# Kernel tuning notes

Measured on AMD Instinct MI355X. Metric: run time of the kernel, lower is better.

## Reference

```python
import jax, jax.numpy as jnp
import numpy as np

B, IN, OUT = 4096, 128, 128
C = 1.0                    # curvature of the Poincare ball
SQRT_C = 1.0
MIN_ENORM = 1e-15          # manifold.min_enorm
BALL_EPS = 1e-5            # projection margin for backproject
EPS32 = float(np.finfo(np.float32).eps)
CLAMP = 1.0 * float(np.log(2.0 / EPS32))   # clamping_factor * log(2/eps)
SMOOTH = 50.0              # smoothing_factor


def _project(y, axis):
    # project back onto the open ball of radius (1 - eps)/sqrt(c)
    norm = jnp.clip(jnp.linalg.norm(y, axis=axis, keepdims=True), MIN_ENORM)
    maxnorm = (1.0 - BALL_EPS) / SQRT_C
    return jnp.where(norm > maxnorm, y * (maxnorm / norm), y)


def _lambda(y, axis):
    # conformal factor lambda(y) = 2 / (1 - c ||y||^2)
    sq = jnp.sum(y * y, axis=axis, keepdims=True)
    return 2.0 / jnp.clip(1.0 - C * sq, EPS32)


def _mobius_add(u, v, axis):
    uv = jnp.sum(u * v, axis=axis, keepdims=True)
    uu = jnp.sum(u * u, axis=axis, keepdims=True)
    vv = jnp.sum(v * v, axis=axis, keepdims=True)
    num = (1.0 + 2.0 * C * uv + C * vv) * u + (1.0 - C * uu) * v
    den = 1.0 + 2.0 * C * uv + (C * C) * uu * vv
    return num / jnp.clip(den, EPS32)


def _smooth_clamp(x, lo, hi, beta):
    # smooth version of clamp; -> hard clamp as beta -> inf
    return lo + (jax.nn.softplus(beta * (x - lo)) - jax.nn.softplus(beta * (x - hi))) / beta


def setup_inputs() -> dict:
    key = jax.random.key(0)
    k1, k2, k3 = jax.random.split(key, 3)
    v = jax.random.normal(k1, (B, IN), dtype=jnp.float32)
    x = 0.7 * v / (1.0 + jnp.linalg.norm(v, axis=-1, keepdims=True))  # strictly inside ball
    weight = jax.random.normal(k2, (OUT, IN), dtype=jnp.float32) * 0.05
    b = jax.random.normal(k3, (OUT, IN), dtype=jnp.float32)
    bias = 0.1 * b / (1.0 + jnp.linalg.norm(b, axis=-1, keepdims=True))  # in-ball translations
    return {"x": x, "weight": weight, "bias": bias}


def reference(x, weight, bias):
    # ptransp_0(weight, bias) = (lambda_0 / lambda_bias) * weight = (1 - c||bias||^2) * weight
    lam_b = _lambda(bias, -1)                       # (out, 1)
    a = (2.0 / lam_b) * weight                      # (out, in) tangent normals at bias
    p = bias                                        # (out, in)

    u = -p.T[None, :, :]                            # (1, in, out)
    v = x[:, :, None]                               # (B, in, 1)
    sub = _mobius_add(u, v, axis=1)                 # (B, in, out) = (-p) (+) x
    sub = _project(sub, axis=1)                     # backproject

    suba = jnp.sum(sub * a.T[None, :, :], axis=1, keepdims=True)         # (B, 1, out)
    a_norm = jnp.clip(jnp.linalg.norm(a, axis=-1, keepdims=True), MIN_ENORM).T  # (1, out)

    asinh_arg = SQRT_C * _lambda(sub, 1) * suba / a_norm[None, :, :]     # (B, 1, out)
    asinh_arg = _smooth_clamp(asinh_arg, -CLAMP, CLAMP, SMOOTH)
    signed_dist = jnp.arcsinh(asinh_arg) / SQRT_C                        # (B, 1, out)

    res = _lambda(p, -1).T * a_norm * signed_dist[:, 0, :]               # (B, out)
    return res
```

## Files before the change

kernel.cpp:

```cpp
#include <hip/hip_runtime.h>
#include <math.h>

#define BB 16
#define NOUT 128
#define NIN 128
#define NTHREADS 256

__global__ __launch_bounds__(NTHREADS) void hyper_kernel(
    const float* __restrict__ x,
    const float* __restrict__ weight,
    const float* __restrict__ bias,
    float* __restrict__ out)
{
    __shared__ __align__(16) float sx[BB][NIN];
    __shared__ float svv[BB];

    const int tid = threadIdx.x;
    const int b0 = blockIdx.x * BB;

    {
        const float4* xg = (const float4*)(x + (size_t)b0 * NIN);
        float4* xs = (float4*)(&sx[0][0]);
        xs[tid] = xg[tid];
        xs[tid + NTHREADS] = xg[tid + NTHREADS];
    }
    __syncthreads();

    if (tid < 128) {
        const int r = tid >> 3, seg = tid & 7;
        float s = 0.f;
        const float4* xr = (const float4*)(&sx[r][seg * 16]);
        #pragma unroll
        for (int j = 0; j < 4; ++j) {
            float4 v = xr[j];
            s = fmaf(v.x, v.x, fmaf(v.y, v.y, fmaf(v.z, v.z, fmaf(v.w, v.w, s))));
        }
        s += __shfl_xor(s, 1);
        s += __shfl_xor(s, 2);
        s += __shfl_xor(s, 4);
        if (seg == 0) svv[r] = s;
    }

    const int o = tid & 127;
    const int rbase = (tid >> 7) * (BB / 2);

    const float4* w4 = (const float4*)(weight + (size_t)o * NIN);
    const float4* b4 = (const float4*)(bias + (size_t)o * NIN);

    float accb[BB / 2], accw[BB / 2];
    #pragma unroll
    for (int r = 0; r < BB / 2; ++r) { accb[r] = 0.f; accw[r] = 0.f; }
    float uu = 0.f, bw = 0.f, ww = 0.f;

    #pragma unroll 4
    for (int kc = 0; kc < NIN / 4; ++kc) {
        const float4 wv = w4[kc];
        const float4 bv = b4[kc];
        uu = fmaf(bv.x, bv.x, uu); uu = fmaf(bv.y, bv.y, uu);
        uu = fmaf(bv.z, bv.z, uu); uu = fmaf(bv.w, bv.w, uu);
        bw = fmaf(bv.x, wv.x, bw); bw = fmaf(bv.y, wv.y, bw);
        bw = fmaf(bv.z, wv.z, bw); bw = fmaf(bv.w, wv.w, bw);
        ww = fmaf(wv.x, wv.x, ww); ww = fmaf(wv.y, wv.y, ww);
        ww = fmaf(wv.z, wv.z, ww); ww = fmaf(wv.w, wv.w, ww);
        #pragma unroll
        for (int r = 0; r < BB / 2; ++r) {
            const float4 xv = *(const float4*)(&sx[rbase + r][kc * 4]);
            accb[r] = fmaf(xv.x, bv.x, accb[r]); accb[r] = fmaf(xv.y, bv.y, accb[r]);
            accb[r] = fmaf(xv.z, bv.z, accb[r]); accb[r] = fmaf(xv.w, bv.w, accb[r]);
            accw[r] = fmaf(xv.x, wv.x, accw[r]); accw[r] = fmaf(xv.y, wv.y, accw[r]);
            accw[r] = fmaf(xv.z, wv.z, accw[r]); accw[r] = fmaf(xv.w, wv.w, accw[r]);
        }
    }
    __syncthreads();

    const float EPS = 1.1920928955078125e-7f;
    const float CLAMPV = 16.635532333438687f;
    const float INV_SMOOTH = 1.f / 50.f;
    const float SMOOTHF = 50.f;
    const float MAXNORM = 1.f - 1e-5f;

    const float beta = 1.f - uu;
    const float beta_c = fmaxf(beta, EPS);
    const float a_norm = fmaxf(beta_c * sqrtf(ww), 1e-15f);
    const float ba = beta_c * bw;
    const float outcoef = (2.f / beta_c) * a_norm;
    const float inv_anorm = 1.f / a_norm;

    #pragma unroll
    for (int r = 0; r < BB / 2; ++r) {
        const float vv = svv[rbase + r];
        const float uv = -accb[r];
        const float dax = beta_c * accw[r];
        const float alpha = 1.f + 2.f * uv + vv;
        const float den = fmaxf(1.f + 2.f * uv + uu * vv, EPS);
        const float inv_den = 1.f / den;
        float suba = (beta * dax - alpha * ba) * inv_den;
        float ss = (alpha * alpha * uu + 2.f * alpha * beta * uv + beta * beta * vv)
                   * (inv_den * inv_den);
        const float nrm = fmaxf(sqrtf(fmaxf(ss, 0.f)), 1e-15f);
        if (nrm > MAXNORM) {
            const float sc = MAXNORM / nrm;
            suba *= sc;
            ss *= sc * sc;
        }
        const float lam_sub = 2.f / fmaxf(1.f - ss, EPS);
        const float arg = lam_sub * suba * inv_anorm;
        const float t1 = SMOOTHF * (arg + CLAMPV);
        const float t2 = SMOOTHF * (arg - CLAMPV);
        const float sp1 = fmaxf(t1, 0.f) + log1pf(expf(-fabsf(t1)));
        const float sp2 = fmaxf(t2, 0.f) + log1pf(expf(-fabsf(t2)));
        const float scl = -CLAMPV + (sp1 - sp2) * INV_SMOOTH;
        const float sd = asinhf(scl);
        out[(size_t)(b0 + rbase + r) * NOUT + o] = outcoef * sd;
    }
}

extern "C" void kernel_launch(void* const* d_in, const int* in_sizes, int n_in,
                              void* d_out, int out_size, void* d_ws, size_t ws_size,
                              hipStream_t stream) {
    const float* x = (const float*)d_in[0];
    const float* w = (const float*)d_in[1];
    const float* b = (const float*)d_in[2];
    float* out = (float*)d_out;
    const int B = in_sizes[0] / NIN;
    dim3 grid(B / BB), block(NTHREADS);
    hipLaunchKernelGGL(hyper_kernel, grid, block, 0, stream, x, w, b, out);
}
```

Baseline: 79.00 us.

## Shrink rows per block, read x via scalar loads, split weight stats across halves

Cuts rows per block from 16 to 4, so the grid grows from 256 to 1024 blocks and fills more compute units. The shared-memory staging of x is dropped: each half-block reads its two x rows straight from global memory through a wave-uniform pointer (readfirstlane), which enables scalar loads. The per-output bias/weight norms are now computed only by the first half and passed through shared memory. The trade-off is that weight and bias are re-read by four times as many blocks, raising L2 traffic in exchange for parallelism and fewer redundant FMAs.

```diff
diff --git a/kernel.cpp b/kernel.cpp
--- a/kernel.cpp
+++ b/kernel.cpp
@@ -1,77 +1,92 @@
 #include <hip/hip_runtime.h>
 #include <math.h>
 
-#define BB 16
+#define NIN 128
 #define NOUT 128
-#define NIN 128
-#define NTHREADS 256
+#define BB 4
+#define NTH 256
 
-__global__ __launch_bounds__(NTHREADS) void hyper_kernel(
+template <bool STATS>
+__device__ __forceinline__ void dot_loop(
+    const float4* __restrict__ w4, const float4* __restrict__ b4,
+    const float* __restrict__ xr0, const float* __restrict__ xr1,
+    float& acb0, float& acw0, float& acb1, float& acw1,
+    float& uu, float& bw, float& ww)
+{
+    #pragma unroll
+    for (int kc = 0; kc < NIN / 4; ++kc) {
+        const float4 wv = w4[kc];
+        const float4 bv = b4[kc];
+        if (STATS) {
+            uu = fmaf(bv.x, bv.x, uu); uu = fmaf(bv.y, bv.y, uu);
+            uu = fmaf(bv.z, bv.z, uu); uu = fmaf(bv.w, bv.w, uu);
+            bw = fmaf(bv.x, wv.x, bw); bw = fmaf(bv.y, wv.y, bw);
+            bw = fmaf(bv.z, wv.z, bw); bw = fmaf(bv.w, wv.w, bw);
+            ww = fmaf(wv.x, wv.x, ww); ww = fmaf(wv.y, wv.y, ww);
+            ww = fmaf(wv.z, wv.z, ww); ww = fmaf(wv.w, wv.w, ww);
+        }
+        const float x00 = xr0[kc * 4 + 0], x01 = xr0[kc * 4 + 1];
+        const float x02 = xr0[kc * 4 + 2], x03 = xr0[kc * 4 + 3];
+        const float x10 = xr1[kc * 4 + 0], x11 = xr1[kc * 4 + 1];
+        const float x12 = xr1[kc * 4 + 2], x13 = xr1[kc * 4 + 3];
+        acb0 = fmaf(x00, bv.x, acb0); acb0 = fmaf(x01, bv.y, acb0);
+        acb0 = fmaf(x02, bv.z, acb0); acb0 = fmaf(x03, bv.w, acb0);
+        acw0 = fmaf(x00, wv.x, acw0); acw0 = fmaf(x01, wv.y, acw0);
+        acw0 = fmaf(x02, wv.z, acw0); acw0 = fmaf(x03, wv.w, acw0);
+        acb1 = fmaf(x10, bv.x, acb1); acb1 = fmaf(x11, bv.y, acb1);
+        acb1 = fmaf(x12, bv.z, acb1); acb1 = fmaf(x13, bv.w, acb1);
+        acw1 = fmaf(x10, wv.x, acw1); acw1 = fmaf(x11, wv.y, acw1);
+        acw1 = fmaf(x12, wv.z, acw1); acw1 = fmaf(x13, wv.w, acw1);
+    }
+}
+
+__global__ __launch_bounds__(NTH) void hyper_kernel(
     const float* __restrict__ x,
     const float* __restrict__ weight,
     const float* __restrict__ bias,
     float* __restrict__ out)
 {
-    __shared__ __align__(16) float sx[BB][NIN];
     __shared__ float svv[BB];
+    __shared__ float s_uu[NOUT];
+    __shared__ float s_bw[NOUT];
+    __shared__ float s_ww[NOUT];
 
     const int tid = threadIdx.x;
     const int b0 = blockIdx.x * BB;
+    const int o = tid & (NOUT - 1);
+    const int rh = tid >> 7;
 
-    {
-        const float4* xg = (const float4*)(x + (size_t)b0 * NIN);
-        float4* xs = (float4*)(&sx[0][0]);
-        xs[tid] = xg[tid];
-        xs[tid + NTHREADS] = xg[tid + NTHREADS];
-    }
-    __syncthreads();
-
-    if (tid < 128) {
-        const int r = tid >> 3, seg = tid & 7;
-        float s = 0.f;
-        const float4* xr = (const float4*)(&sx[r][seg * 16]);
-        #pragma unroll
-        for (int j = 0; j < 4; ++j) {
-            float4 v = xr[j];
-            s = fmaf(v.x, v.x, fmaf(v.y, v.y, fmaf(v.z, v.z, fmaf(v.w, v.w, s))));
-        }
+    if (tid < 32 * BB) {
+        const int r = tid >> 5, seg = tid & 31;
+        const float4 v = *(const float4*)(x + (size_t)(b0 + r) * NIN + seg * 4);
+        float s = fmaf(v.x, v.x, fmaf(v.y, v.y, fmaf(v.z, v.z, v.w * v.w)));
         s += __shfl_xor(s, 1);
         s += __shfl_xor(s, 2);
         s += __shfl_xor(s, 4);
+        s += __shfl_xor(s, 8);
+        s += __shfl_xor(s, 16);
         if (seg == 0) svv[r] = s;
     }
 
-    const int o = tid & 127;
-    const int rbase = (tid >> 7) * (BB / 2);
-
+    const int row0 = b0 + rh * 2;
+    const float* xr0 = x + (size_t)((unsigned)__builtin_amdgcn_readfirstlane(row0)) * NIN;
+    const float* xr1 = xr0 + NIN;
     const float4* w4 = (const float4*)(weight + (size_t)o * NIN);
     const float4* b4 = (const float4*)(bias + (size_t)o * NIN);
 
-    float accb[BB / 2], accw[BB / 2];
-    #pragma unroll
-    for (int r = 0; r < BB / 2; ++r) { accb[r] = 0.f; accw[r] = 0.f; }
+    float acb0 = 0.f, acw0 = 0.f, acb1 = 0.f, acw1 = 0.f;
     float uu = 0.f, bw = 0.f, ww = 0.f;
 
-    #pragma unroll 4
-    for (int kc = 0; kc < NIN / 4; ++kc) {
-        const float4 wv = w4[kc];
-        const float4 bv = b4[kc];
-        uu = fmaf(bv.x, bv.x, uu); uu = fmaf(bv.y, bv.y, uu);
-        uu = fmaf(bv.z, bv.z, uu); uu = fmaf(bv.w, bv.w, uu);
-        bw = fmaf(bv.x, wv.x, bw); bw = fmaf(bv.y, wv.y, bw);
-        bw = fmaf(bv.z, wv.z, bw); bw = fmaf(bv.w, wv.w, bw);
-        ww = fmaf(wv.x, wv.x, ww); ww = fmaf(wv.y, wv.y, ww);
-        ww = fmaf(wv.z, wv.z, ww); ww = fmaf(wv.w, wv.w, ww);
-        #pragma unroll
-        for (int r = 0; r < BB / 2; ++r) {
-            const float4 xv = *(const float4*)(&sx[rbase + r][kc * 4]);
-            accb[r] = fmaf(xv.x, bv.x, accb[r]); accb[r] = fmaf(xv.y, bv.y, accb[r]);
-            accb[r] = fmaf(xv.z, bv.z, accb[r]); accb[r] = fmaf(xv.w, bv.w, accb[r]);
-            accw[r] = fmaf(xv.x, wv.x, accw[r]); accw[r] = fmaf(xv.y, wv.y, accw[r]);
-            accw[r] = fmaf(xv.z, wv.z, accw[r]); accw[r] = fmaf(xv.w, wv.w, accw[r]);
-        }
+    if (rh == 0) {
+        dot_loop<true>(w4, b4, xr0, xr1, acb0, acw0, acb1, acw1, uu, bw, ww);
+        s_uu[o] = uu; s_bw[o] = bw; s_ww[o] = ww;
+    } else {
+        dot_loop<false>(w4, b4, xr0, xr1, acb0, acw0, acb1, acw1, uu, bw, ww);
     }
     __syncthreads();
+    uu = s_uu[o]; bw = s_bw[o]; ww = s_ww[o];
+    const float vv0 = svv[rh * 2 + 0];
+    const float vv1 = svv[rh * 2 + 1];
 
     const float EPS = 1.1920928955078125e-7f;
     const float CLAMPV = 16.635532333438687f;
@@ -86,9 +101,13 @@
     const float outcoef = (2.f / beta_c) * a_norm;
     const float inv_anorm = 1.f / a_norm;
 
+    float accb[2] = {acb0, acb1};
+    float accw[2] = {acw0, acw1};
+    float vvs[2] = {vv0, vv1};
+
     #pragma unroll
-    for (int r = 0; r < BB / 2; ++r) {
-        const float vv = svv[rbase + r];
+    for (int r = 0; r < 2; ++r) {
+        const float vv = vvs[r];
         const float uv = -accb[r];
         const float dax = beta_c * accw[r];
         const float alpha = 1.f + 2.f * uv + vv;
@@ -111,7 +130,7 @@
         const float sp2 = fmaxf(t2, 0.f) + log1pf(expf(-fabsf(t2)));
         const float scl = -CLAMPV + (sp1 - sp2) * INV_SMOOTH;
         const float sd = asinhf(scl);
-        out[(size_t)(b0 + rbase + r) * NOUT + o] = outcoef * sd;
+        out[(size_t)(row0 + r) * NOUT + o] = outcoef * sd;
     }
 }
 
@@ -123,6 +142,6 @@
     const float* b = (const float*)d_in[2];
     float* out = (float*)d_out;
     const int B = in_sizes[0] / NIN;
-    dim3 grid(B / BB), block(NTHREADS);
+    dim3 grid(B / BB), block(NTH);
     hipLaunchKernelGGL(hyper_kernel, grid, block, 0, stream, x, w, b, out);
 }
```

After: 101.7 us. 1.29x slower.

## Split K across 16-lane groups with DPP reductions and spread epilogue across lanes

Applied to the files above, without the earlier changes.

Restructures the kernel so that each 16-lane group owns one output column. The 128-wide dot products are split across the 16 lanes, 8 elements each, and summed with DPP row-rotate reductions. The transcendental-heavy epilogue is then distributed so each lane handles a different row, instead of one thread doing every row serially. Shared memory staging is removed: x is read straight from global memory and hits L2 repeatedly across the 8 column blocks. The grid grows to 1024 blocks. The cost is much more redundant global/L2 traffic for x and the extra reduction instructions.

```diff
diff --git a/kernel.cpp b/kernel.cpp
--- a/kernel.cpp
+++ b/kernel.cpp
@@ -1,84 +1,98 @@
 #include <hip/hip_runtime.h>
 #include <math.h>
 
-#define BB 16
+#define NIN 128
 #define NOUT 128
-#define NIN 128
-#define NTHREADS 256
+#define ROWS_PER_BLOCK 32
+#define COLS_PER_BLOCK 16
+#define NTH 256
 
-__global__ __launch_bounds__(NTHREADS) void hyper_kernel(
-    const float* __restrict__ x,
-    const float* __restrict__ weight,
-    const float* __restrict__ bias,
-    float* __restrict__ out)
+template <int N>
+__device__ __forceinline__ float row_ror(float v) {
+    return __int_as_float(__builtin_amdgcn_update_dpp(
+        0, __float_as_int(v), 0x120 + N, 0xF, 0xF, true));
+}
+
+__device__ __forceinline__ float red16(float v) {
+    v += row_ror<1>(v);
+    v += row_ror<2>(v);
+    v += row_ror<4>(v);
+    v += row_ror<8>(v);
+    return v;
+}
+
+__device__ __forceinline__ float dot8(float4 a0, float4 a1, float4 b0, float4 b1) {
+    float s = a0.x * b0.x;
+    s = fmaf(a0.y, b0.y, s);
+    s = fmaf(a0.z, b0.z, s);
+    s = fmaf(a0.w, b0.w, s);
+    s = fmaf(a1.x, b1.x, s);
+    s = fmaf(a1.y, b1.y, s);
+    s = fmaf(a1.z, b1.z, s);
+    s = fmaf(a1.w, b1.w, s);
+    return s;
+}
+
+__device__ __forceinline__ float epilogue(
+    float uv, float xw, float vv,
+    float uu, float beta, float beta_c, float ba,
+    float inv_anorm, float outcoef)
 {
-    __shared__ __align__(16) float sx[BB][NIN];
-    __shared__ float svv[BB];
-
-    const int tid = threadIdx.x;
-    const int b0 = blockIdx.x * BB;
-
-    {
-        const float4* xg = (const float4*)(x + (size_t)b0 * NIN);
-        float4* xs = (float4*)(&sx[0][0]);
-        xs[tid] = xg[tid];
-        xs[tid + NTHREADS] = xg[tid + NTHREADS];
-    }
-    __syncthreads();
-
-    if (tid < 128) {
-        const int r = tid >> 3, seg = tid & 7;
-        float s = 0.f;
-        const float4* xr = (const float4*)(&sx[r][seg * 16]);
-        #pragma unroll
-        for (int j = 0; j < 4; ++j) {
-            float4 v = xr[j];
-            s = fmaf(v.x, v.x, fmaf(v.y, v.y, fmaf(v.z, v.z, fmaf(v.w, v.w, s))));
-        }
-        s += __shfl_xor(s, 1);
-        s += __shfl_xor(s, 2);
-        s += __shfl_xor(s, 4);
-        if (seg == 0) svv[r] = s;
-    }
-
-    const int o = tid & 127;
-    const int rbase = (tid >> 7) * (BB / 2);
-
-    const float4* w4 = (const float4*)(weight + (size_t)o * NIN);
-    const float4* b4 = (const float4*)(bias + (size_t)o * NIN);
-
-    float accb[BB / 2], accw[BB / 2];
-    #pragma unroll
-    for (int r = 0; r < BB / 2; ++r) { accb[r] = 0.f; accw[r] = 0.f; }
-    float uu = 0.f, bw = 0.f, ww = 0.f;
-
-    #pragma unroll 4
-    for (int kc = 0; kc < NIN / 4; ++kc) {
-        const float4 wv = w4[kc];
-        const float4 bv = b4[kc];
-        uu = fmaf(bv.x, bv.x, uu); uu = fmaf(bv.y, bv.y, uu);
-        uu = fmaf(bv.z, bv.z, uu); uu = fmaf(bv.w, bv.w, uu);
-        bw = fmaf(bv.x, wv.x, bw); bw = fmaf(bv.y, wv.y, bw);
-        bw = fmaf(bv.z, wv.z, bw); bw = fmaf(bv.w, wv.w, bw);
-        ww = fmaf(wv.x, wv.x, ww); ww = fmaf(wv.y, wv.y, ww);
-        ww = fmaf(wv.z, wv.z, ww); ww = fmaf(wv.w, wv.w, ww);
-        #pragma unroll
-        for (int r = 0; r < BB / 2; ++r) {
-            const float4 xv = *(const float4*)(&sx[rbase + r][kc * 4]);
-            accb[r] = fmaf(xv.x, bv.x, accb[r]); accb[r] = fmaf(xv.y, bv.y, accb[r]);
-            accb[r] = fmaf(xv.z, bv.z, accb[r]); accb[r] = fmaf(xv.w, bv.w, accb[r]);
-            accw[r] = fmaf(xv.x, wv.x, accw[r]); accw[r] = fmaf(xv.y, wv.y, accw[r]);
-            accw[r] = fmaf(xv.z, wv.z, accw[r]); accw[r] = fmaf(xv.w, wv.w, accw[r]);
-        }
-    }
-    __syncthreads();
-
     const float EPS = 1.1920928955078125e-7f;
     const float CLAMPV = 16.635532333438687f;
     const float INV_SMOOTH = 1.f / 50.f;
     const float SMOOTHF = 50.f;
     const float MAXNORM = 1.f - 1e-5f;
 
+    const float dax = beta_c * xw;
+    const float alpha = 1.f + 2.f * uv + vv;
+    const float den = fmaxf(1.f + 2.f * uv + uu * vv, EPS);
+    const float inv_den = 1.f / den;
+    float suba = (beta * dax - alpha * ba) * inv_den;
+    float ss = (alpha * alpha * uu + 2.f * alpha * beta * uv + beta * beta * vv)
+               * (inv_den * inv_den);
+    const float nrm = fmaxf(sqrtf(fmaxf(ss, 0.f)), 1e-15f);
+    if (nrm > MAXNORM) {
+        const float sc = MAXNORM / nrm;
+        suba *= sc;
+        ss *= sc * sc;
+    }
+    const float lam_sub = 2.f / fmaxf(1.f - ss, EPS);
+    const float arg = lam_sub * suba * inv_anorm;
+    const float t1 = SMOOTHF * (arg + CLAMPV);
+    const float t2 = SMOOTHF * (arg - CLAMPV);
+    const float sp1 = fmaxf(t1, 0.f) + log1pf(expf(-fabsf(t1)));
+    const float sp2 = fmaxf(t2, 0.f) + log1pf(expf(-fabsf(t2)));
+    const float scl = -CLAMPV + (sp1 - sp2) * INV_SMOOTH;
+    return outcoef * asinhf(scl);
+}
+
+__global__ __launch_bounds__(NTH) void hyper_kernel(
+    const float* __restrict__ x,
+    const float* __restrict__ weight,
+    const float* __restrict__ bias,
+    float* __restrict__ out)
+{
+    const int tid = threadIdx.x;
+    const int wave = tid >> 6;
+    const int lane = tid & 63;
+    const int g = lane >> 4;
+    const int t = lane & 15;
+    const int blk_col = blockIdx.x & 7;
+    const int blk_row = blockIdx.x >> 3;
+    const int o = blk_col * COLS_PER_BLOCK + wave * 4 + g;
+    const int rb = blk_row * ROWS_PER_BLOCK;
+
+    const float4* wp = (const float4*)(weight + (size_t)o * NIN + t * 8);
+    const float4* bp = (const float4*)(bias + (size_t)o * NIN + t * 8);
+    const float4 wr0 = wp[0], wr1 = wp[1];
+    const float4 br0 = bp[0], br1 = bp[1];
+
+    const float uu = red16(dot8(br0, br1, br0, br1));
+    const float bw = red16(dot8(br0, br1, wr0, wr1));
+    const float ww = red16(dot8(wr0, wr1, wr0, wr1));
+
+    const float EPS = 1.1920928955078125e-7f;
     const float beta = 1.f - uu;
     const float beta_c = fmaxf(beta, EPS);
     const float a_norm = fmaxf(beta_c * sqrtf(ww), 1e-15f);
@@ -86,32 +100,27 @@
     const float outcoef = (2.f / beta_c) * a_norm;
     const float inv_anorm = 1.f / a_norm;
 
+    const float* xbase = x + (size_t)rb * NIN + t * 8;
+
     #pragma unroll
-    for (int r = 0; r < BB / 2; ++r) {
-        const float vv = svv[rbase + r];
-        const float uv = -accb[r];
-        const float dax = beta_c * accw[r];
-        const float alpha = 1.f + 2.f * uv + vv;
-        const float den = fmaxf(1.f + 2.f * uv + uu * vv, EPS);
-        const float inv_den = 1.f / den;
-        float suba = (beta * dax - alpha * ba) * inv_den;
-        float ss = (alpha * alpha * uu + 2.f * alpha * beta * uv + beta * beta * vv)
-                   * (inv_den * inv_den);
-        const float nrm = fmaxf(sqrtf(fmaxf(ss, 0.f)), 1e-15f);
-        if (nrm > MAXNORM) {
-            const float sc = MAXNORM / nrm;
-            suba *= sc;
-            ss *= sc * sc;
+    for (int c = 0; c < ROWS_PER_BLOCK / 16; ++c) {
+        float uvK = 0.f, xwK = 0.f, vvK = 0.f;
+        #pragma unroll 4
+        for (int r = 0; r < 16; ++r) {
+            const float4* xp = (const float4*)(xbase + (size_t)(c * 16 + r) * NIN);
+            const float4 xv0 = xp[0];
+            const float4 xv1 = xp[1];
+            float pb = dot8(xv0, xv1, br0, br1);
+            float pw = dot8(xv0, xv1, wr0, wr1);
+            float pv = dot8(xv0, xv1, xv0, xv1);
+            pb = red16(pb);
+            pw = red16(pw);
+            pv = red16(pv);
+            if (t == r) { uvK = -pb; xwK = pw; vvK = pv; }
         }
-        const float lam_sub = 2.f / fmaxf(1.f - ss, EPS);
-        const float arg = lam_sub * suba * inv_anorm;
-        const float t1 = SMOOTHF * (arg + CLAMPV);
-        const float t2 = SMOOTHF * (arg - CLAMPV);
-        const float sp1 = fmaxf(t1, 0.f) + log1pf(expf(-fabsf(t1)));
-        const float sp2 = fmaxf(t2, 0.f) + log1pf(expf(-fabsf(t2)));
-        const float scl = -CLAMPV + (sp1 - sp2) * INV_SMOOTH;
-        const float sd = asinhf(scl);
-        out[(size_t)(b0 + rbase + r) * NOUT + o] = outcoef * sd;
+        const float val = epilogue(uvK, xwK, vvK, uu, beta, beta_c, ba,
+                                   inv_anorm, outcoef);
+        out[(size_t)(rb + c * 16 + t) * NOUT + o] = val;
     }
 }
 
@@ -123,6 +132,6 @@
     const float* b = (const float*)d_in[2];
     float* out = (float*)d_out;
     const int B = in_sizes[0] / NIN;
-    dim3 grid(B / BB), block(NTHREADS);
+    dim3 grid((NOUT / COLS_PER_BLOCK) * (B / ROWS_PER_BLOCK)), block(NTH);
     hipLaunchKernelGGL(hyper_kernel, grid, block, 0, stream, x, w, b, out);
 }
```

Measured after the change: 77.98 us. No clear change (-1.3%).

## Use split-bf16 MFMA for x·W and x·b dot products with a prep kernel

Applied to the files above, without the earlier changes.

Adds a prep kernel that splits x, weight and bias into bf16 hi/lo pairs and precomputes the row norms of x and the per-output-column constants. The main kernel then computes x·W and x·b with 16x16x32 bf16 MFMA, using three products (hi·hi, hi·lo, lo·hi) to approximate fp32 accuracy, and runs the same elementwise hyperbolic epilogue as before. This replaces the scalar FMA inner loop and the redundant per-block recomputation of the bias and weight norms. It costs a second kernel launch, extra workspace traffic, and a small accuracy loss from the three-term split.

```diff
diff --git a/kernel.cpp b/kernel.cpp
--- a/kernel.cpp
+++ b/kernel.cpp
@@ -1,96 +1,135 @@
 #include <hip/hip_runtime.h>
 #include <math.h>
 
-#define BB 16
+typedef __attribute__((ext_vector_type(8))) short short8;
+typedef __attribute__((ext_vector_type(4))) float floatx4;
+
+#define NIN 128
 #define NOUT 128
-#define NIN 128
-#define NTHREADS 256
 
-__global__ __launch_bounds__(NTHREADS) void hyper_kernel(
-    const float* __restrict__ x,
-    const float* __restrict__ weight,
-    const float* __restrict__ bias,
+__device__ __forceinline__ unsigned short f2bf(float f) {
+    unsigned u = __float_as_uint(f);
+    unsigned r = (u + 0x7fffu + ((u >> 16) & 1u)) >> 16;
+    return (unsigned short)r;
+}
+__device__ __forceinline__ float bf2f(unsigned short h) {
+    return __uint_as_float(((unsigned)h) << 16);
+}
+
+__global__ __launch_bounds__(256) void hyper_prep(
+    const float* __restrict__ x, const float* __restrict__ w,
+    const float* __restrict__ bia,
+    unsigned short* __restrict__ xhi, unsigned short* __restrict__ xlo,
+    unsigned short* __restrict__ whi, unsigned short* __restrict__ wlo,
+    unsigned short* __restrict__ bhi, unsigned short* __restrict__ blo,
+    float* __restrict__ vvp, float* __restrict__ colc)
+{
+    const int wave = threadIdx.x >> 6;
+    const int lane = threadIdx.x & 63;
+    if (blockIdx.x < 1024) {
+        const int row = blockIdx.x * 4 + wave;
+        const float2 v = *(const float2*)(x + (size_t)row * NIN + lane * 2);
+        const unsigned short h0 = f2bf(v.x), h1 = f2bf(v.y);
+        ushort2 hh; hh.x = h0; hh.y = h1;
+        ushort2 ll; ll.x = f2bf(v.x - bf2f(h0)); ll.y = f2bf(v.y - bf2f(h1));
+        *(ushort2*)(xhi + (size_t)row * NIN + lane * 2) = hh;
+        *(ushort2*)(xlo + (size_t)row * NIN + lane * 2) = ll;
+        float s = fmaf(v.x, v.x, v.y * v.y);
+        #pragma unroll
+        for (int m = 1; m < 64; m <<= 1) s += __shfl_xor(s, m);
+        if (lane == 0) vvp[row] = s;
+    } else {
+        const int col = (blockIdx.x - 1024) * 4 + wave;
+        const size_t base = (size_t)col * NIN;
+        const float w0 = w[base + lane], w1 = w[base + 64 + lane];
+        const float b0 = bia[base + lane], b1 = bia[base + 64 + lane];
+        const unsigned short wh0 = f2bf(w0), wh1 = f2bf(w1);
+        const unsigned short bh0 = f2bf(b0), bh1 = f2bf(b1);
+        whi[base + lane] = wh0;            whi[base + 64 + lane] = wh1;
+        wlo[base + lane] = f2bf(w0 - bf2f(wh0)); wlo[base + 64 + lane] = f2bf(w1 - bf2f(wh1));
+        bhi[base + lane] = bh0;            bhi[base + 64 + lane] = bh1;
+        blo[base + lane] = f2bf(b0 - bf2f(bh0)); blo[base + 64 + lane] = f2bf(b1 - bf2f(bh1));
+        float uu = fmaf(b0, b0, b1 * b1);
+        float bw = fmaf(b0, w0, b1 * w1);
+        float ww = fmaf(w0, w0, w1 * w1);
+        #pragma unroll
+        for (int m = 1; m < 64; m <<= 1) {
+            uu += __shfl_xor(uu, m);
+            bw += __shfl_xor(bw, m);
+            ww += __shfl_xor(ww, m);
+        }
+        if (lane == 0) {
+            const float EPS = 1.1920928955078125e-7f;
+            const float beta = 1.f - uu;
+            const float beta_c = fmaxf(beta, EPS);
+            const float a_norm = fmaxf(beta_c * sqrtf(ww), 1e-15f);
+            float4 c;
+            c.x = uu;
+            c.y = beta_c * bw;
+            c.z = 1.f / a_norm;
+            c.w = (2.f / beta_c) * a_norm;
+            *(float4*)(colc + (size_t)col * 4) = c;
+        }
+    }
+}
+
+__global__ __launch_bounds__(256) void hyper_main(
+    const unsigned short* __restrict__ xhi, const unsigned short* __restrict__ xlo,
+    const unsigned short* __restrict__ whi, const unsigned short* __restrict__ wlo,
+    const unsigned short* __restrict__ bhi, const unsigned short* __restrict__ blo,
+    const float* __restrict__ vvp, const float* __restrict__ colc,
     float* __restrict__ out)
 {
-    __shared__ __align__(16) float sx[BB][NIN];
-    __shared__ float svv[BB];
+    const int wave = threadIdx.x >> 6;
+    const int lane = threadIdx.x & 63;
+    const int q = lane >> 4, i = lane & 15;
+    const int m0 = (blockIdx.x >> 1) * 16;
+    const int n0 = ((blockIdx.x & 1) * 4 + wave) * 16;
 
-    const int tid = threadIdx.x;
-    const int b0 = blockIdx.x * BB;
+    const size_t abase = (size_t)(m0 + i) * NIN + q * 8;
+    const size_t bbase = (size_t)(n0 + i) * NIN + q * 8;
 
-    {
-        const float4* xg = (const float4*)(x + (size_t)b0 * NIN);
-        float4* xs = (float4*)(&sx[0][0]);
-        xs[tid] = xg[tid];
-        xs[tid + NTHREADS] = xg[tid + NTHREADS];
-    }
-    __syncthreads();
-
-    if (tid < 128) {
-        const int r = tid >> 3, seg = tid & 7;
-        float s = 0.f;
-        const float4* xr = (const float4*)(&sx[r][seg * 16]);
-        #pragma unroll
-        for (int j = 0; j < 4; ++j) {
-            float4 v = xr[j];
-            s = fmaf(v.x, v.x, fmaf(v.y, v.y, fmaf(v.z, v.z, fmaf(v.w, v.w, s))));
-        }
-        s += __shfl_xor(s, 1);
-        s += __shfl_xor(s, 2);
-        s += __shfl_xor(s, 4);
-        if (seg == 0) svv[r] = s;
+    short8 ah[4], al[4], wh[4], wl[4], bh[4], bl[4];
+    #pragma unroll
+    for (int kc = 0; kc < 4; ++kc) {
+        ah[kc] = *(const short8*)(xhi + abase + kc * 32);
+        al[kc] = *(const short8*)(xlo + abase + kc * 32);
+        wh[kc] = *(const short8*)(whi + bbase + kc * 32);
+        wl[kc] = *(const short8*)(wlo + bbase + kc * 32);
+        bh[kc] = *(const short8*)(bhi + bbase + kc * 32);
+        bl[kc] = *(const short8*)(blo + bbase + kc * 32);
     }
 
-    const int o = tid & 127;
-    const int rbase = (tid >> 7) * (BB / 2);
+    floatx4 accW1 = {0.f, 0.f, 0.f, 0.f}, accW2 = {0.f, 0.f, 0.f, 0.f};
+    floatx4 accB1 = {0.f, 0.f, 0.f, 0.f}, accB2 = {0.f, 0.f, 0.f, 0.f};
+    #pragma unroll
+    for (int kc = 0; kc < 4; ++kc) {
+        accW1 = __builtin_amdgcn_mfma_f32_16x16x32_bf16(ah[kc], wh[kc], accW1, 0, 0, 0);
+        accB1 = __builtin_amdgcn_mfma_f32_16x16x32_bf16(ah[kc], bh[kc], accB1, 0, 0, 0);
+        accW2 = __builtin_amdgcn_mfma_f32_16x16x32_bf16(ah[kc], wl[kc], accW2, 0, 0, 0);
+        accB2 = __builtin_amdgcn_mfma_f32_16x16x32_bf16(ah[kc], bl[kc], accB2, 0, 0, 0);
+        accW2 = __builtin_amdgcn_mfma_f32_16x16x32_bf16(al[kc], wh[kc], accW2, 0, 0, 0);
+        accB2 = __builtin_amdgcn_mfma_f32_16x16x32_bf16(al[kc], bh[kc], accB2, 0, 0, 0);
+    }
 
-    const float4* w4 = (const float4*)(weight + (size_t)o * NIN);
-    const float4* b4 = (const float4*)(bias + (size_t)o * NIN);
-
-    float accb[BB / 2], accw[BB / 2];
-    #pragma unroll
-    for (int r = 0; r < BB / 2; ++r) { accb[r] = 0.f; accw[r] = 0.f; }
-    float uu = 0.f, bw = 0.f, ww = 0.f;
-
-    #pragma unroll 4
-    for (int kc = 0; kc < NIN / 4; ++kc) {
-        const float4 wv = w4[kc];
-        const float4 bv = b4[kc];
-        uu = fmaf(bv.x, bv.x, uu); uu = fmaf(bv.y, bv.y, uu);
-        uu = fmaf(bv.z, bv.z, uu); uu = fmaf(bv.w, bv.w, uu);
-        bw = fmaf(bv.x, wv.x, bw); bw = fmaf(bv.y, wv.y, bw);
-        bw = fmaf(bv.z, wv.z, bw); bw = fmaf(bv.w, wv.w, bw);
-        ww = fmaf(wv.x, wv.x, ww); ww = fmaf(wv.y, wv.y, ww);
-        ww = fmaf(wv.z, wv.z, ww); ww = fmaf(wv.w, wv.w, ww);
-        #pragma unroll
-        for (int r = 0; r < BB / 2; ++r) {
-            const float4 xv = *(const float4*)(&sx[rbase + r][kc * 4]);
-            accb[r] = fmaf(xv.x, bv.x, accb[r]); accb[r] = fmaf(xv.y, bv.y, accb[r]);
-            accb[r] = fmaf(xv.z, bv.z, accb[r]); accb[r] = fmaf(xv.w, bv.w, accb[r]);
-            accw[r] = fmaf(xv.x, wv.x, accw[r]); accw[r] = fmaf(xv.y, wv.y, accw[r]);
-            accw[r] = fmaf(xv.z, wv.z, accw[r]); accw[r] = fmaf(xv.w, wv.w, accw[r]);
-        }
-    }
-    __syncthreads();
+    const float4 cc = *(const float4*)(colc + (size_t)(n0 + i) * 4);
+    const float uu = cc.x, ba = cc.y, inv_anorm = cc.z, outcoef = cc.w;
 
     const float EPS = 1.1920928955078125e-7f;
     const float CLAMPV = 16.635532333438687f;
     const float INV_SMOOTH = 1.f / 50.f;
     const float SMOOTHF = 50.f;
     const float MAXNORM = 1.f - 1e-5f;
-
     const float beta = 1.f - uu;
     const float beta_c = fmaxf(beta, EPS);
-    const float a_norm = fmaxf(beta_c * sqrtf(ww), 1e-15f);
-    const float ba = beta_c * bw;
-    const float outcoef = (2.f / beta_c) * a_norm;
-    const float inv_anorm = 1.f / a_norm;
 
     #pragma unroll
-    for (int r = 0; r < BB / 2; ++r) {
-        const float vv = svv[rbase + r];
-        const float uv = -accb[r];
-        const float dax = beta_c * accw[r];
+    for (int r = 0; r < 4; ++r) {
+        const int row = m0 + q * 4 + r;
+        const float vv = vvp[row];
+        const float uv = -(accB1[r] + accB2[r]);
+        const float xw = accW1[r] + accW2[r];
+        const float dax = beta_c * xw;
         const float alpha = 1.f + 2.f * uv + vv;
         const float den = fmaxf(1.f + 2.f * uv + uu * vv, EPS);
         const float inv_den = 1.f / den;
@@ -110,8 +149,7 @@
         const float sp1 = fmaxf(t1, 0.f) + log1pf(expf(-fabsf(t1)));
         const float sp2 = fmaxf(t2, 0.f) + log1pf(expf(-fabsf(t2)));
         const float scl = -CLAMPV + (sp1 - sp2) * INV_SMOOTH;
-        const float sd = asinhf(scl);
-        out[(size_t)(b0 + rbase + r) * NOUT + o] = outcoef * sd;
+        out[(size_t)row * NOUT + n0 + i] = outcoef * asinhf(scl);
     }
 }
 
@@ -122,7 +160,18 @@
     const float* w = (const float*)d_in[1];
     const float* b = (const float*)d_in[2];
     float* out = (float*)d_out;
-    const int B = in_sizes[0] / NIN;
-    dim3 grid(B / BB), block(NTHREADS);
-    hipLaunchKernelGGL(hyper_kernel, grid, block, 0, stream, x, w, b, out);
+
+    unsigned short* xhi = (unsigned short*)d_ws;
+    unsigned short* xlo = xhi + 524288;
+    unsigned short* whi = xlo + 524288;
+    unsigned short* wlo = whi + 16384;
+    unsigned short* bhi = wlo + 16384;
+    unsigned short* blo = bhi + 16384;
+    float* vvp = (float*)(blo + 16384);
+    float* colc = vvp + 4096;
+
+    hipLaunchKernelGGL(hyper_prep, dim3(1056), dim3(256), 0, stream,
+                       x, w, b, xhi, xlo, whi, wlo, bhi, blo, vvp, colc);
+    hipLaunchKernelGGL(hyper_main, dim3(512), dim3(256), 0, stream,
+                       xhi, xlo, whi, wlo, bhi, blo, vvp, colc, out);
 }
```

Measured after the change: 73.11 us. 7.5% less time.
